# Kernel tuning notes

Measured on AMD Instinct MI355X. Metric: run time of the kernel, lower is better.

## Reference

```python
import jax, jax.numpy as jnp
import numpy as np

D = 1024
H = 16
T_BLOCK = 2048


def setup_inputs() -> dict:
    key = jax.random.key(0)
    ks = jax.random.split(key, 12)
    B, T = 2, 2048
    s = lambda k, shape: jax.random.normal(k, shape, jnp.float32) * 0.02
    return {
        "x": jax.random.normal(ks[0], (B, T, D), jnp.float32),
        # layernorms
        "ln1_g": jnp.ones((D,), jnp.float32), "ln1_b": jnp.zeros((D,), jnp.float32),
        "ln2_g": jnp.ones((D,), jnp.float32), "ln2_b": jnp.zeros((D,), jnp.float32),
        # attention qkv projection ([in,out] layout) and output proj
        "w_qkv": s(ks[1], (D, 3 * D)), "b_qkv": jnp.zeros((3 * D,), jnp.float32),
        "w_o": s(ks[2], (D, D)), "b_o": jnp.zeros((D,), jnp.float32),
        # MLP
        "w_fc1": s(ks[3], (D, 4 * D)), "b_fc1": jnp.zeros((4 * D,), jnp.float32),
        "w_fc2": s(ks[4], (4 * D, D)), "b_fc2": jnp.zeros((D,), jnp.float32),
    }


def _layernorm(x, g, b, eps=1e-5):
    mu = jnp.mean(x, axis=-1, keepdims=True)
    var = jnp.var(x, axis=-1, keepdims=True)
    return (x - mu) * jax.lax.rsqrt(var + eps) * g + b


def _attention(x, w_qkv, b_qkv, w_o, b_o):
    B, T, C = x.shape
    hd = C // H
    qkv = x @ w_qkv + b_qkv                      # [B,T,3C]
    q, k, v = jnp.split(qkv, 3, axis=-1)
    split = lambda t: t.reshape(B, T, H, hd).transpose(0, 2, 1, 3)  # [B,H,T,hd]
    q, k, v = split(q), split(k), split(v)
    att = jnp.einsum("bhqd,bhkd->bhqk", q, k) / jnp.sqrt(jnp.float32(hd))
    causal = jnp.tril(jnp.ones((T, T), bool))
    att = jnp.where(causal[None, None], att, -jnp.inf)
    att = jax.nn.softmax(att, axis=-1)
    y = jnp.einsum("bhqk,bhkd->bhqd", att, v)    # [B,H,T,hd]
    y = y.transpose(0, 2, 1, 3).reshape(B, T, C)
    return y @ w_o + b_o


def reference(x, ln1_g, ln1_b, ln2_g, ln2_b, w_qkv, b_qkv, w_o, b_o,
              w_fc1, b_fc1, w_fc2, b_fc2):
    # dropout is identity in eval mode
    x = x + _attention(_layernorm(x, ln1_g, ln1_b), w_qkv, b_qkv, w_o, b_o)
    h = jax.nn.gelu(_layernorm(x, ln2_g, ln2_b) @ w_fc1 + b_fc1)
    return x + (h @ w_fc2 + b_fc2)
```

## Files before the change

kernel.cpp:

```cpp
#include <hip/hip_runtime.h>
#include <hip/hip_bf16.h>


using bf16 = __bf16;
using bf16x8 = __attribute__((ext_vector_type(8))) __bf16;
using floatx4 = __attribute__((ext_vector_type(4))) float;

#define D_ 1024
#define T_ 2048
#define B_ 2
#define H_ 16

static __device__ __forceinline__ bf16 f2bf(float f) { return (bf16)f; }

static __device__ __forceinline__ void async16(const void* g, void* l) {
  __builtin_amdgcn_global_load_lds(
      (const __attribute__((address_space(1))) void*)g,
      (__attribute__((address_space(3))) void*)l, 16, 0, 0);
}

static __device__ __forceinline__ float gelu_f(float v) {
  const float u2 = 1.5957691216057308f * (v + 0.044715f * v * v * v);
  return v / (1.0f + __expf(-u2));
}

__global__ void transpose_cast(const float* __restrict__ in, bf16* __restrict__ out,
                               int K, int N) {
  __shared__ float tile[32][33];
  const int n0 = blockIdx.x * 32, k0 = blockIdx.y * 32;
  const int tx = threadIdx.x, ty = threadIdx.y;
  for (int i = 0; i < 32; i += 8)
    tile[ty + i][tx] = in[(size_t)(k0 + ty + i) * N + n0 + tx];
  __syncthreads();
  for (int i = 0; i < 32; i += 8)
    out[(size_t)(n0 + ty + i) * K + k0 + tx] = f2bf(tile[tx][ty + i]);
}

__global__ __launch_bounds__(256)
void ln_kernel(const float* __restrict__ x, const float* __restrict__ g,
               const float* __restrict__ bsh, bf16* __restrict__ out) {
  const int row = blockIdx.x, tid = threadIdx.x;
  const float4 v = ((const float4*)(x + (size_t)row * D_))[tid];
  float s = v.x + v.y + v.z + v.w;
  float s2 = v.x * v.x + v.y * v.y + v.z * v.z + v.w * v.w;
  for (int off = 32; off; off >>= 1) {
    s += __shfl_xor(s, off);
    s2 += __shfl_xor(s2, off);
  }
  __shared__ float red[8];
  const int wave = tid >> 6, lane = tid & 63;
  if (lane == 0) { red[wave] = s; red[wave + 4] = s2; }
  __syncthreads();
  s = red[0] + red[1] + red[2] + red[3];
  s2 = red[4] + red[5] + red[6] + red[7];
  const float mu = s * (1.0f / D_);
  const float rstd = rsqrtf(s2 * (1.0f / D_) - mu * mu + 1e-5f);
  const float4 gv = ((const float4*)g)[tid];
  const float4 bv = ((const float4*)bsh)[tid];
  bf16 o[4] __attribute__((aligned(8)));
  o[0] = f2bf((v.x - mu) * rstd * gv.x + bv.x);
  o[1] = f2bf((v.y - mu) * rstd * gv.y + bv.y);
  o[2] = f2bf((v.z - mu) * rstd * gv.z + bv.z);
  o[3] = f2bf((v.w - mu) * rstd * gv.w + bv.w);
  *(ushort4*)(out + (size_t)row * D_ + tid * 4) = *(const ushort4*)o;
}

template <int EPI>
__global__ __launch_bounds__(256)
void gemm_bt(const bf16* __restrict__ A, const bf16* __restrict__ Bt,
             const float* __restrict__ bias, const float* __restrict__ res,
             void* __restrict__ Cout, int M, int N, int K) {
  __shared__ __align__(16) bf16 As[2][128][64];
  __shared__ __align__(16) bf16 Bs[2][128][64];
  const int tid = threadIdx.x;
  const int wave = tid >> 6, lane = tid & 63;
  const int quad = lane >> 4, l16 = lane & 15;
  const int wr = wave >> 1, wc = wave & 1;
  const int bm = blockIdx.x * 128, bn = blockIdx.y * 128;
  const int lrow8 = lane >> 3;
  const int lcol = (((lane & 7) ^ lrow8) * 8);

  const bf16* aBase = &A[(size_t)(bm + wave * 32 + lrow8) * K + lcol];
  const bf16* bBase = &Bt[(size_t)(bn + wave * 32 + lrow8) * K + lcol];

  auto stage = [&](int buf, int kk) {
    const int k0 = kk * 64;
    for (int c = 0; c < 4; c++) {
      async16(aBase + (size_t)c * 8 * K + k0, &As[buf][wave * 32 + c * 8][0]);
      async16(bBase + (size_t)c * 8 * K + k0, &Bs[buf][wave * 32 + c * 8][0]);
    }
  };

  floatx4 acc[4][4] = {};
  const int nsteps = K >> 6;

  stage(0, 0);
  if (nsteps > 1) stage(1, 1);
  int cur = 0;
  for (int t = 0; t < nsteps; ++t) {
    if (t < nsteps - 1)
      asm volatile("s_waitcnt vmcnt(8)" ::: "memory");
    else
      asm volatile("s_waitcnt vmcnt(0)" ::: "memory");
    __builtin_amdgcn_s_barrier();
    __builtin_amdgcn_sched_barrier(0);
    for (int ks = 0; ks < 2; ks++) {
      const int fc = ((quad + ks * 4) ^ (l16 & 7)) * 8;
      bf16x8 af[4], bfr[4];
      for (int mt = 0; mt < 4; mt++)
        af[mt] = *(const bf16x8*)&As[cur][wr * 64 + mt * 16 + l16][fc];
      for (int nn = 0; nn < 4; nn++)
        bfr[nn] = *(const bf16x8*)&Bs[cur][wc * 64 + nn * 16 + l16][fc];
      for (int mt = 0; mt < 4; mt++)
        for (int nn = 0; nn < 4; nn++)
          acc[mt][nn] = __builtin_amdgcn_mfma_f32_16x16x32_bf16(
              af[mt], bfr[nn], acc[mt][nn], 0, 0, 0);
    }
    __builtin_amdgcn_sched_barrier(0);
    __builtin_amdgcn_s_barrier();
    if (t + 2 < nsteps) stage(cur, t + 2);
    cur ^= 1;
  }

  for (int mt = 0; mt < 4; mt++) {
    for (int nn = 0; nn < 4; nn++) {
      const int col = bn + wc * 64 + nn * 16 + l16;
      const float bcol = bias[col];
      for (int i = 0; i < 4; i++) {
        const int row = bm + wr * 64 + mt * 16 + quad * 4 + i;
        float v = acc[mt][nn][i] + bcol;
        if (EPI == 0) {
          ((bf16*)Cout)[(size_t)row * N + col] = f2bf(v);
        } else if (EPI == 1) {
          ((bf16*)Cout)[(size_t)row * N + col] = f2bf(gelu_f(v));
        } else {
          ((float*)Cout)[(size_t)row * N + col] = v + res[(size_t)row * N + col];
        }
      }
    }
  }
}

template <int EPI>
__global__ __launch_bounds__(256)
void gemm64_k128(const bf16* __restrict__ A, const bf16* __restrict__ Bt,
                 const float* __restrict__ bias, const float* __restrict__ res,
                 void* __restrict__ Cout, int M, int N, int K) {
  __shared__ __align__(16) bf16 As[64][128];
  __shared__ __align__(16) bf16 Bs[128][128];
  const int tid = threadIdx.x;
  const int wave = tid >> 6, lane = tid & 63;
  const int quad = lane >> 4, l16 = lane & 15;
  const int wr = wave >> 1, wc = wave & 1;
  const int bm = blockIdx.x * 64, bn = blockIdx.y * 128;
  const int sr = lane >> 4;
  const int pchunk = lane & 15;

  floatx4 acc[2][4] = {};

  for (int k0 = 0; k0 < K; k0 += 128) {
    __syncthreads();
    for (int c = 0; c < 4; c++) {
      const int base = wave * 16 + c * 4;
      const int scol = (pchunk ^ ((c * 4 + sr) & 15)) * 8;
      async16(&A[(size_t)(bm + base + sr) * K + k0 + scol], &As[base][0]);
    }
    for (int c = 0; c < 8; c++) {
      const int base = wave * 32 + c * 4;
      const int scol = (pchunk ^ ((c * 4 + sr) & 15)) * 8;
      async16(&Bt[(size_t)(bn + base + sr) * K + k0 + scol], &Bs[base][0]);
    }
    __syncthreads();
    for (int ks = 0; ks < 4; ks++) {
      const int fc = ((quad + ks * 4) ^ l16) * 8;
      bf16x8 af[2], bfr[4];
      for (int mt = 0; mt < 2; mt++)
        af[mt] = *(const bf16x8*)&As[wr * 32 + mt * 16 + l16][fc];
      for (int nt = 0; nt < 4; nt++)
        bfr[nt] = *(const bf16x8*)&Bs[wc * 64 + nt * 16 + l16][fc];
      for (int mt = 0; mt < 2; mt++)
        for (int nt = 0; nt < 4; nt++)
          acc[mt][nt] = __builtin_amdgcn_mfma_f32_16x16x32_bf16(
              af[mt], bfr[nt], acc[mt][nt], 0, 0, 0);
    }
  }

  for (int mt = 0; mt < 2; mt++) {
    for (int nt = 0; nt < 4; nt++) {
      const int col = bn + wc * 64 + nt * 16 + l16;
      const float bcol = bias[col];
      for (int i = 0; i < 4; i++) {
        const int row = bm + wr * 32 + mt * 16 + quad * 4 + i;
        float v = acc[mt][nt][i] + bcol;
        if (EPI == 0) {
          ((bf16*)Cout)[(size_t)row * N + col] = f2bf(v);
        } else if (EPI == 1) {
          ((bf16*)Cout)[(size_t)row * N + col] = f2bf(gelu_f(v));
        } else {
          ((float*)Cout)[(size_t)row * N + col] = v + res[(size_t)row * N + col];
        }
      }
    }
  }
}

__global__ __launch_bounds__(512)
void attn_kernel(const bf16* __restrict__ qkv, bf16* __restrict__ y) {
  const int bh = blockIdx.y, b = bh >> 4, h = bh & 15;
  const int tile = (blockIdx.y & 16) ? (int)blockIdx.x : (15 - (int)blockIdx.x);
  const int q0 = tile * 128;
  const int tid = threadIdx.x, wave = tid >> 6, lane = tid & 63;
  const int quad = lane >> 4, l16 = lane & 15;
  const int l7 = l16 & 7;
  const int w16 = wave * 16;

  __shared__ __align__(16) bf16 Ks[64][64];
  __shared__ __align__(16) bf16 Vts[64][64];
  __shared__ __align__(16) bf16 Ps[128][64];

  const size_t bbase = (size_t)b * T_ * 3072 + (size_t)h * 64;
  const bf16* Qg = qkv + bbase;
  const bf16* Kg = qkv + bbase + 1024;
  const bf16* Vg = qkv + bbase + 2048;

  bf16x8 ones;
  for (int j = 0; j < 8; j++) ones[j] = f2bf(1.0f);

  const int kr = tid >> 3, kch = tid & 7;
  const int kcol = ((kch ^ (kr & 7)) * 8);
  const int vk = tid & 63, vd = tid >> 6;

  bf16x8 qf[2];
  for (int ks = 0; ks < 2; ks++) {
    bf16x8 t = *(const bf16x8*)
        &Qg[(size_t)(q0 + w16 + l16) * 3072 + ks * 32 + quad * 8];
    for (int j = 0; j < 8; j++) t[j] = f2bf((float)t[j] * 0.125f);
    qf[ks] = t;
  }

  int4 kreg = *(const int4*)&Kg[(size_t)kr * 3072 + kch * 8];
  bf16x8 vreg = *(const bf16x8*)&Vg[(size_t)vk * 3072 + vd * 8];

  floatx4 accY[4] = {};
  floatx4 accL = {};

  const int kend = q0 + 64;
  for (int kc = 0; kc <= kend; kc += 64) {
    __syncthreads();
    *(int4*)&Ks[kr][kcol] = kreg;
    for (int j = 0; j < 8; j++) {
      const int d = vd * 8 + j;
      Vts[d][((vk >> 3) ^ j) * 8 + (vk & 7)] = vreg[j];
    }
    __syncthreads();

    if (kc < kend) {
      kreg = *(const int4*)&Kg[(size_t)(kc + 64 + kr) * 3072 + kch * 8];
      vreg = *(const bf16x8*)&Vg[(size_t)(kc + 64 + vk) * 3072 + vd * 8];
    }

    floatx4 s[4];
    for (int nt = 0; nt < 4; nt++) {
      const bf16* krow = &Ks[nt * 16 + l16][0];
      bf16x8 kf0 = *(const bf16x8*)&krow[(quad ^ l7) * 8];
      bf16x8 kf1 = *(const bf16x8*)&krow[((4 + quad) ^ l7) * 8];
      floatx4 t = {};
      t = __builtin_amdgcn_mfma_f32_16x16x32_bf16(qf[0], kf0, t, 0, 0, 0);
      t = __builtin_amdgcn_mfma_f32_16x16x32_bf16(qf[1], kf1, t, 0, 0, 0);
      s[nt] = t;
    }
    if (kc + 64 > q0 + w16) {
      for (int nt = 0; nt < 4; nt++)
        for (int i = 0; i < 4; i++) {
          const int c = kc + nt * 16 + l16;
          const int r = q0 + w16 + quad * 4 + i;
          if (c > r) s[nt][i] = -1e30f;
        }
    }

    for (int i = 0; i < 4; i++) {
      const int pr = quad * 4 + i;
      bf16* prow = &Ps[w16 + pr][0];
      for (int nt = 0; nt < 4; nt++)
        prow[(((nt * 2 + (l16 >> 3)) ^ (pr & 7)) * 8) + l7] =
            f2bf(__expf(s[nt][i] - 8.0f));
    }
    __builtin_amdgcn_wave_barrier();

    for (int ks = 0; ks < 2; ks++) {
      bf16x8 pa = *(const bf16x8*)&Ps[w16 + l16][((ks * 4 + quad) ^ l7) * 8];
      for (int dt = 0; dt < 4; dt++) {
        bf16x8 vb = *(const bf16x8*)&Vts[dt * 16 + l16][((ks * 4 + quad) ^ l7) * 8];
        accY[dt] =
            __builtin_amdgcn_mfma_f32_16x16x32_bf16(pa, vb, accY[dt], 0, 0, 0);
      }
      accL = __builtin_amdgcn_mfma_f32_16x16x32_bf16(pa, ones, accL, 0, 0, 0);
    }
  }

  for (int i = 0; i < 4; i++) {
    const float linv = 1.0f / accL[i];
    const int r = q0 + w16 + quad * 4 + i;
    for (int dt = 0; dt < 4; dt++)
      y[(size_t)(b * T_ + r) * D_ + h * 64 + dt * 16 + l16] =
          f2bf(accY[dt][i] * linv);
  }
}

extern "C" void kernel_launch(void* const* d_in, const int* in_sizes, int n_in,
                              void* d_out, int out_size, void* d_ws, size_t ws_size,
                              hipStream_t stream) {
  const float* x     = (const float*)d_in[0];
  const float* ln1_g = (const float*)d_in[1];
  const float* ln1_b = (const float*)d_in[2];
  const float* ln2_g = (const float*)d_in[3];
  const float* ln2_b = (const float*)d_in[4];
  const float* w_qkv = (const float*)d_in[5];
  const float* b_qkv = (const float*)d_in[6];
  const float* w_o   = (const float*)d_in[7];
  const float* b_o   = (const float*)d_in[8];
  const float* w_fc1 = (const float*)d_in[9];
  const float* b_fc1 = (const float*)d_in[10];
  const float* w_fc2 = (const float*)d_in[11];
  const float* b_fc2 = (const float*)d_in[12];

  char* p = (char*)d_ws;
  bf16* wqkvT = (bf16*)p; p += (size_t)3072 * 1024 * 2;
  bf16* woT   = (bf16*)p; p += (size_t)1024 * 1024 * 2;
  bf16* wfc1T = (bf16*)p; p += (size_t)4096 * 1024 * 2;
  bf16* wfc2T = (bf16*)p; p += (size_t)1024 * 4096 * 2;
  bf16* ln1   = (bf16*)p; p += (size_t)4096 * 1024 * 2;
  bf16* qkv   = (bf16*)p; p += (size_t)4096 * 3072 * 2;
  bf16* yb    = (bf16*)p; p += (size_t)4096 * 1024 * 2;
  float* x2   = (float*)p; p += (size_t)4096 * 1024 * 4;
  bf16* ln2   = (bf16*)p; p += (size_t)4096 * 1024 * 2;
  bf16* hb    = (bf16*)p; p += (size_t)4096 * 4096 * 2;

  const dim3 tb(32, 8);
  transpose_cast<<<dim3(96, 32), tb, 0, stream>>>(w_qkv, wqkvT, 1024, 3072);
  transpose_cast<<<dim3(32, 32), tb, 0, stream>>>(w_o, woT, 1024, 1024);
  transpose_cast<<<dim3(128, 32), tb, 0, stream>>>(w_fc1, wfc1T, 1024, 4096);
  transpose_cast<<<dim3(32, 128), tb, 0, stream>>>(w_fc2, wfc2T, 4096, 1024);

  ln_kernel<<<4096, 256, 0, stream>>>(x, ln1_g, ln1_b, ln1);
  gemm_bt<0><<<dim3(32, 24), 256, 0, stream>>>(ln1, wqkvT, b_qkv, nullptr, qkv,
                                               4096, 3072, 1024);
  attn_kernel<<<dim3(16, 32), 512, 0, stream>>>(qkv, yb);
  gemm64_k128<2><<<dim3(64, 8), 256, 0, stream>>>(yb, woT, b_o, x, x2,
                                                  4096, 1024, 1024);
  ln_kernel<<<4096, 256, 0, stream>>>(x2, ln2_g, ln2_b, ln2);
  gemm_bt<1><<<dim3(32, 32), 256, 0, stream>>>(ln2, wfc1T, b_fc1, nullptr, hb,
                                               4096, 4096, 1024);
  gemm64_k128<2><<<dim3(64, 8), 256, 0, stream>>>(hb, wfc2T, b_fc2, x2, (float*)d_out,
                                                  4096, 1024, 4096);
}
```

Baseline: 319.1 us.

## Double-buffer the 64-row GEMM and use single-buffered kernel for QKV projection

Replaces the single-buffered K=128 64x128 GEMM (used for the output and fc2 projections) with a double-buffered K=64 version. It prefetches two stages ahead with async global-to-LDS loads and explicit vmcnt waits, so loads overlap the MFMA work. It also adds a single-buffered 128x128 GEMM variant for the QKV projection, which halves LDS use and may raise occupancy. The risks are that the hand-counted vmcnt values must match the number of outstanding loads, and that the QKV kernel loses load/compute overlap.

New measurement: 331.5 us. 1.04x slower.

```diff
diff --git a/kernel.cpp b/kernel.cpp
--- a/kernel.cpp
+++ b/kernel.cpp
@@ -63,6 +63,64 @@
   o[2] = f2bf((v.z - mu) * rstd * gv.z + bv.z);
   o[3] = f2bf((v.w - mu) * rstd * gv.w + bv.w);
   *(ushort4*)(out + (size_t)row * D_ + tid * 4) = *(const ushort4*)o;
+}
+
+template <int EPI>
+__global__ __launch_bounds__(256)
+void gemm_bt_sb(const bf16* __restrict__ A, const bf16* __restrict__ Bt,
+                const float* __restrict__ bias, const float* __restrict__ res,
+                void* __restrict__ Cout, int M, int N, int K) {
+  __shared__ __align__(16) bf16 As[128][64];
+  __shared__ __align__(16) bf16 Bs[128][64];
+  const int tid = threadIdx.x;
+  const int wave = tid >> 6, lane = tid & 63;
+  const int quad = lane >> 4, l16 = lane & 15;
+  const int wr = wave >> 1, wc = wave & 1;
+  const int bm = blockIdx.x * 128, bn = blockIdx.y * 128;
+  const int lrow8 = lane >> 3;
+  const int lcol = (((lane & 7) ^ lrow8) * 8);
+
+  floatx4 acc[4][4] = {};
+
+  for (int k0 = 0; k0 < K; k0 += 64) {
+    __syncthreads();
+    for (int c = 0; c < 4; c++) {
+      const int r = wave * 32 + c * 8;
+      async16(&A[(size_t)(bm + r + lrow8) * K + k0 + lcol], &As[r][0]);
+      async16(&Bt[(size_t)(bn + r + lrow8) * K + k0 + lcol], &Bs[r][0]);
+    }
+    __syncthreads();
+    for (int ks = 0; ks < 2; ks++) {
+      const int fc = ((quad + ks * 4) ^ (l16 & 7)) * 8;
+      bf16x8 af[4], bfr[4];
+      for (int mt = 0; mt < 4; mt++)
+        af[mt] = *(const bf16x8*)&As[wr * 64 + mt * 16 + l16][fc];
+      for (int nt = 0; nt < 4; nt++)
+        bfr[nt] = *(const bf16x8*)&Bs[wc * 64 + nt * 16 + l16][fc];
+      for (int mt = 0; mt < 4; mt++)
+        for (int nt = 0; nt < 4; nt++)
+          acc[mt][nt] = __builtin_amdgcn_mfma_f32_16x16x32_bf16(
+              af[mt], bfr[nt], acc[mt][nt], 0, 0, 0);
+    }
+  }
+
+  for (int mt = 0; mt < 4; mt++) {
+    for (int nt = 0; nt < 4; nt++) {
+      const int col = bn + wc * 64 + nt * 16 + l16;
+      const float bcol = bias[col];
+      for (int i = 0; i < 4; i++) {
+        const int row = bm + wr * 64 + mt * 16 + quad * 4 + i;
+        float v = acc[mt][nt][i] + bcol;
+        if (EPI == 0) {
+          ((bf16*)Cout)[(size_t)row * N + col] = f2bf(v);
+        } else if (EPI == 1) {
+          ((bf16*)Cout)[(size_t)row * N + col] = f2bf(gelu_f(v));
+        } else {
+          ((float*)Cout)[(size_t)row * N + col] = v + res[(size_t)row * N + col];
+        }
+      }
+    }
+  }
 }
 
 template <int EPI>
@@ -143,46 +201,59 @@
 
 template <int EPI>
 __global__ __launch_bounds__(256)
-void gemm64_k128(const bf16* __restrict__ A, const bf16* __restrict__ Bt,
+void gemm64_dbuf(const bf16* __restrict__ A, const bf16* __restrict__ Bt,
                  const float* __restrict__ bias, const float* __restrict__ res,
                  void* __restrict__ Cout, int M, int N, int K) {
-  __shared__ __align__(16) bf16 As[64][128];
-  __shared__ __align__(16) bf16 Bs[128][128];
+  __shared__ __align__(16) bf16 As[2][64][64];
+  __shared__ __align__(16) bf16 Bs[2][128][64];
   const int tid = threadIdx.x;
   const int wave = tid >> 6, lane = tid & 63;
   const int quad = lane >> 4, l16 = lane & 15;
   const int wr = wave >> 1, wc = wave & 1;
   const int bm = blockIdx.x * 64, bn = blockIdx.y * 128;
-  const int sr = lane >> 4;
-  const int pchunk = lane & 15;
+  const int lrow8 = lane >> 3;
+  const int lcol = (((lane & 7) ^ lrow8) * 8);
+
+  const bf16* aBase = &A[(size_t)(bm + wave * 16 + lrow8) * K + lcol];
+  const bf16* bBase = &Bt[(size_t)(bn + wave * 32 + lrow8) * K + lcol];
+
+  auto stage = [&](int buf, int kk) {
+    const int k0 = kk * 64;
+    for (int c = 0; c < 2; c++)
+      async16(aBase + (size_t)c * 8 * K + k0, &As[buf][wave * 16 + c * 8][0]);
+    for (int c = 0; c < 4; c++)
+      async16(bBase + (size_t)c * 8 * K + k0, &Bs[buf][wave * 32 + c * 8][0]);
+  };
 
   floatx4 acc[2][4] = {};
-
-  for (int k0 = 0; k0 < K; k0 += 128) {
-    __syncthreads();
-    for (int c = 0; c < 4; c++) {
-      const int base = wave * 16 + c * 4;
-      const int scol = (pchunk ^ ((c * 4 + sr) & 15)) * 8;
-      async16(&A[(size_t)(bm + base + sr) * K + k0 + scol], &As[base][0]);
-    }
-    for (int c = 0; c < 8; c++) {
-      const int base = wave * 32 + c * 4;
-      const int scol = (pchunk ^ ((c * 4 + sr) & 15)) * 8;
-      async16(&Bt[(size_t)(bn + base + sr) * K + k0 + scol], &Bs[base][0]);
-    }
-    __syncthreads();
-    for (int ks = 0; ks < 4; ks++) {
-      const int fc = ((quad + ks * 4) ^ l16) * 8;
+  const int nsteps = K >> 6;
+
+  stage(0, 0);
+  if (nsteps > 1) stage(1, 1);
+  int cur = 0;
+  for (int t = 0; t < nsteps; ++t) {
+    if (t < nsteps - 1)
+      asm volatile("s_waitcnt vmcnt(6)" ::: "memory");
+    else
+      asm volatile("s_waitcnt vmcnt(0)" ::: "memory");
+    __builtin_amdgcn_s_barrier();
+    __builtin_amdgcn_sched_barrier(0);
+    for (int ks = 0; ks < 2; ks++) {
+      const int fc = ((quad + ks * 4) ^ (l16 & 7)) * 8;
       bf16x8 af[2], bfr[4];
       for (int mt = 0; mt < 2; mt++)
-        af[mt] = *(const bf16x8*)&As[wr * 32 + mt * 16 + l16][fc];
+        af[mt] = *(const bf16x8*)&As[cur][wr * 32 + mt * 16 + l16][fc];
       for (int nt = 0; nt < 4; nt++)
-        bfr[nt] = *(const bf16x8*)&Bs[wc * 64 + nt * 16 + l16][fc];
+        bfr[nt] = *(const bf16x8*)&Bs[cur][wc * 64 + nt * 16 + l16][fc];
       for (int mt = 0; mt < 2; mt++)
         for (int nt = 0; nt < 4; nt++)
           acc[mt][nt] = __builtin_amdgcn_mfma_f32_16x16x32_bf16(
               af[mt], bfr[nt], acc[mt][nt], 0, 0, 0);
     }
+    __builtin_amdgcn_sched_barrier(0);
+    __builtin_amdgcn_s_barrier();
+    if (t + 2 < nsteps) stage(cur, t + 2);
+    cur ^= 1;
   }
 
   for (int mt = 0; mt < 2; mt++) {
@@ -343,14 +414,14 @@
   transpose_cast<<<dim3(32, 128), tb, 0, stream>>>(w_fc2, wfc2T, 4096, 1024);
 
   ln_kernel<<<4096, 256, 0, stream>>>(x, ln1_g, ln1_b, ln1);
-  gemm_bt<0><<<dim3(32, 24), 256, 0, stream>>>(ln1, wqkvT, b_qkv, nullptr, qkv,
-                                               4096, 3072, 1024);
+  gemm_bt_sb<0><<<dim3(32, 24), 256, 0, stream>>>(ln1, wqkvT, b_qkv, nullptr, qkv,
+                                                  4096, 3072, 1024);
   attn_kernel<<<dim3(16, 32), 512, 0, stream>>>(qkv, yb);
-  gemm64_k128<2><<<dim3(64, 8), 256, 0, stream>>>(yb, woT, b_o, x, x2,
+  gemm64_dbuf<2><<<dim3(64, 8), 256, 0, stream>>>(yb, woT, b_o, x, x2,
                                                   4096, 1024, 1024);
   ln_kernel<<<4096, 256, 0, stream>>>(x2, ln2_g, ln2_b, ln2);
   gemm_bt<1><<<dim3(32, 32), 256, 0, stream>>>(ln2, wfc1T, b_fc1, nullptr, hb,
                                                4096, 4096, 1024);
-  gemm64_k128<2><<<dim3(64, 8), 256, 0, stream>>>(hb, wfc2T, b_fc2, x2, (float*)d_out,
+  gemm64_dbuf<2><<<dim3(64, 8), 256, 0, stream>>>(hb, wfc2T, b_fc2, x2, (float*)d_out,
                                                   4096, 1024, 4096);
 }
```
